# Kernel tuning notes

Measured on AMD Instinct MI355X. Metric: run time of the kernel, lower is better.

The kernel has to match this reference:

```python
import jax, jax.numpy as jnp
import numpy as np

B, T, C, H = 4096, 4, 1024, 8
DH = C // H
SCALE = DH ** -0.5
LN_EPS = 1e-5


def setup_inputs() -> dict:
    key = jax.random.key(0)
    k1, k2, k3 = jax.random.split(key, 3)
    feats = jax.random.normal(k1, (B, T, C), dtype=jnp.float32)
    Wqkv = jax.random.normal(k2, (T, C, 3 * C), dtype=jnp.float32) * 0.02
    bqkv = jnp.zeros((T, 3 * C), dtype=jnp.float32)
    Wproj = jax.random.normal(k3, (T, C, C), dtype=jnp.float32) * 0.02
    bproj = jnp.zeros((T, C), dtype=jnp.float32)
    gamma = jnp.ones((C,), dtype=jnp.float32)
    beta = jnp.zeros((C,), dtype=jnp.float32)
    return {"feats": feats, "Wqkv": Wqkv, "bqkv": bqkv,
            "Wproj": Wproj, "bproj": bproj, "gamma": gamma, "beta": beta}


def reference(feats, Wqkv, bqkv, Wproj, bproj, gamma, beta):
    # Grouped per-task QKV projection: [B,T,C] x [T,C,3C] -> [B,T,3C]
    qkv = jnp.einsum('btc,tcd->btd', feats, Wqkv) + bqkv
    q, k, v = jnp.split(qkv, 3, axis=-1)           # each [B,T,C]
    q = q.reshape(B, T, H, DH)
    k = k.reshape(B, T, H, DH)
    v = v.reshape(B, T, H, DH)
    # Cross-task attention: scores[b, query_task, key_task, head]
    scores = jnp.einsum('bqhd,bkhd->bqkh', q, k) * SCALE
    attn = jax.nn.softmax(scores, axis=2)          # softmax over key-task dim
    ctx = jnp.einsum('bqkh,bkhd->bqhd', attn, v)   # [B,T,H,DH]
    ctx = ctx.reshape(B, T, C)
    # Grouped per-task output projection (dropout is identity in eval)
    ctx = jnp.einsum('btc,tcd->btd', ctx, Wproj) + bproj
    # Residual + shared LayerNorm over channel dim
    x = ctx + feats
    mu = jnp.mean(x, axis=-1, keepdims=True)
    var = jnp.mean(jnp.square(x - mu), axis=-1, keepdims=True)
    return (x - mu) * jax.lax.rsqrt(var + LN_EPS) * gamma + beta
```

## Files before the change

### kernel.cpp

```cpp
#include <hip/hip_runtime.h>
#include <hip/hip_bf16.h>
#include <cstdint>
#include <cstddef>

#define B_SZ 4096
#define T_SZ 4
#define C_SZ 1024
#define H_SZ 8
#define DH_SZ 128
#define NQKV 3072
#define SCALE_F 0.08838834764831845f

typedef float f32x4 __attribute__((ext_vector_type(4)));
typedef short s16x8 __attribute__((ext_vector_type(8)));

static __device__ __forceinline__ float bf2f(unsigned short u) {
    union { unsigned int i; float f; } x; x.i = ((unsigned int)u) << 16; return x.f;
}
static __device__ __forceinline__ unsigned short f2bf(float f) {
    union { unsigned int i; float f; } x; x.f = f;
    unsigned int r = x.i + 0x7FFFu + ((x.i >> 16) & 1u);
    return (unsigned short)(r >> 16);
}

typedef const __attribute__((address_space(1))) void* gas_ptr;
typedef __attribute__((address_space(3))) void* las_ptr;
static __device__ __forceinline__ void async16(const void* g, void* l) {
    __builtin_amdgcn_global_load_lds((gas_ptr)g, (las_ptr)l, 16, 0, 0);
}

__global__ __launch_bounds__(256) void cvt_f32_bf16(const float* __restrict__ src,
                                                    unsigned short* __restrict__ dst, int n4) {
    int stride = gridDim.x * 256;
    for (int i = blockIdx.x * 256 + threadIdx.x; i < n4; i += stride) {
        float4 v = reinterpret_cast<const float4*>(src)[i];
        ushort4 o;
        o.x = f2bf(v.x); o.y = f2bf(v.y); o.z = f2bf(v.z); o.w = f2bf(v.w);
        reinterpret_cast<ushort4*>(dst)[i] = o;
    }
}

__global__ __launch_bounds__(256) void transpose_cvt(const float* __restrict__ src,
                                                     unsigned short* __restrict__ dst,
                                                     int K, int N) {
    __shared__ float tile[64][33];
    const float* s = src + (size_t)blockIdx.z * K * N;
    unsigned short* d = dst + (size_t)blockIdx.z * K * N;
    int n0 = blockIdx.x * 32, k0 = blockIdx.y * 64;
    int tx = threadIdx.x, ty = threadIdx.y;
#pragma unroll
    for (int i = 0; i < 8; i++) {
        int k = k0 + ty + i * 8;
        tile[ty + i * 8][tx] = s[(size_t)k * N + n0 + tx];
    }
    __syncthreads();
#pragma unroll
    for (int i = 0; i < 4; i++) {
        int n = n0 + ty + i * 8;
        ushort2 o;
        o.x = f2bf(tile[2 * tx][ty + i * 8]);
        o.y = f2bf(tile[2 * tx + 1][ty + i * 8]);
        *reinterpret_cast<ushort2*>(&d[(size_t)n * K + k0 + 2 * tx]) = o;
    }
}

template<int NSIZE>
__global__ __launch_bounds__(512, 1) void gemm256(
    const unsigned short* __restrict__ A,
    const unsigned short* __restrict__ Bt,
    const float* __restrict__ bias,
    unsigned short* __restrict__ out_bf)
{
    constexpr int BK  = 64;
    constexpr int NBX = NSIZE / 256;
    constexpr int NBY = B_SZ / 256;
    constexpr int NWG = NBX * NBY * T_SZ;

    __shared__ __align__(16) unsigned short lds[65536];

    const int bid = blockIdx.x;
    const int swz = (bid & 7) * (NWG >> 3) + (bid >> 3);
    const int by  = swz & (NBY - 1);
    const int tmp = swz >> 4;
    const int bx  = tmp % NBX;
    const int t   = tmp / NBX;
    const int m0  = by * 256;
    const int n0  = bx * 256;

    const int tid  = threadIdx.x;
    const int lane = tid & 63;
    const int w    = tid >> 6;
    const int wm   = w >> 2;
    const int wn   = w & 3;
    const int quad = lane >> 4;
    const int l16  = lane & 15;

    const int q0  = w * 128 + lane;
    const int q1  = q0 + 64;
    const int r0  = q0 >> 3, ch0 = (q0 & 7) ^ (r0 & 7);
    const int r1  = q1 >> 3, ch1 = (q1 & 7) ^ (r1 & 7);
    const unsigned short* Abase = A + (size_t)t * C_SZ;
    const unsigned short* Bbase = Bt + (size_t)t * NSIZE * C_SZ;
    const unsigned short* gA0 = Abase + (size_t)(m0 + r0) * (T_SZ * C_SZ) + ch0 * 8;
    const unsigned short* gA1 = Abase + (size_t)(m0 + r1) * (T_SZ * C_SZ) + ch1 * 8;
    const unsigned short* gB0 = Bbase + (size_t)(n0 + r0) * C_SZ + ch0 * 8;
    const unsigned short* gB1 = Bbase + (size_t)(n0 + r1) * C_SZ + ch1 * 8;
    unsigned short* dA0 = &lds[(w * 2 + 0) * 512];
    unsigned short* dA1 = &lds[(w * 2 + 1) * 512];
    unsigned short* dB0 = &lds[32768 + (w * 2 + 0) * 512];
    unsigned short* dB1 = &lds[32768 + (w * 2 + 1) * 512];

#define STG_A(buf, h, kt) do { \
    async16(gA0 + (size_t)(h) * 128 * (T_SZ * C_SZ) + (kt) * BK, dA0 + (buf) * 16384 + (h) * 8192); \
    async16(gA1 + (size_t)(h) * 128 * (T_SZ * C_SZ) + (kt) * BK, dA1 + (buf) * 16384 + (h) * 8192); \
} while (0)
#define STG_B(buf, h, kt) do { \
    async16(gB0 + (size_t)(h) * 128 * C_SZ + (kt) * BK, dB0 + (buf) * 16384 + (h) * 8192); \
    async16(gB1 + (size_t)(h) * 128 * C_SZ + (kt) * BK, dB1 + (buf) * 16384 + (h) * 8192); \
} while (0)

    const int s7   = l16 & 7;
    const int swk0 = ((0 * 4 + quad) ^ s7) * 8;
    const int swk1 = ((1 * 4 + quad) ^ s7) * 8;
    const unsigned short* aR = &lds[wm * 8192 + l16 * 64];
    const unsigned short* bR = &lds[32768 + (wn >> 1) * 8192 + ((wn & 1) * 64 + l16) * 64];

#define LD_A(buf, mh) do { \
    _Pragma("unroll") \
    for (int mi = 0; mi < 4; ++mi) { \
        af[mi][0] = *(const s16x8*)(aR + (buf) * 16384 + ((mh) * 4 + mi) * 1024 + swk0); \
        af[mi][1] = *(const s16x8*)(aR + (buf) * 16384 + ((mh) * 4 + mi) * 1024 + swk1); \
    } \
} while (0)
#define LD_B(buf, nh, dst) do { \
    _Pragma("unroll") \
    for (int ni = 0; ni < 2; ++ni) { \
        dst[ni][0] = *(const s16x8*)(bR + (buf) * 16384 + ((nh) * 2 + ni) * 1024 + swk0); \
        dst[ni][1] = *(const s16x8*)(bR + (buf) * 16384 + ((nh) * 2 + ni) * 1024 + swk1); \
    } \
} while (0)
#define MM(mh, nh, bsrc) do { \
    _Pragma("unroll") \
    for (int mi = 0; mi < 4; ++mi) \
    _Pragma("unroll") \
    for (int ni = 0; ni < 2; ++ni) { \
        acc[(mh) * 4 + mi][(nh) * 2 + ni] = __builtin_amdgcn_mfma_f32_16x16x32_bf16( \
            af[mi][0], bsrc[ni][0], acc[(mh) * 4 + mi][(nh) * 2 + ni], 0, 0, 0); \
        acc[(mh) * 4 + mi][(nh) * 2 + ni] = __builtin_amdgcn_mfma_f32_16x16x32_bf16( \
            af[mi][1], bsrc[ni][1], acc[(mh) * 4 + mi][(nh) * 2 + ni], 0, 0, 0); \
    } \
} while (0)
#define WALL() do { \
    __builtin_amdgcn_s_barrier(); \
    __builtin_amdgcn_sched_barrier(0); \
} while (0)
#define KTILE(buf, kt, SP0, SP23, VMC) do { \
     \
    asm volatile("s_waitcnt vmcnt(" #VMC ")"); \
    __builtin_amdgcn_sched_barrier(0); \
    WALL(); \
    LD_B(buf, 0, bq0); \
    LD_A(buf, 0); \
    LD_B(buf, 1, bq1); \
    if (SP0) STG_A((buf) ^ 1, 1, (kt) + 1); \
    __builtin_amdgcn_s_setprio(1); MM(0, 0, bq0); MM(0, 1, bq1); __builtin_amdgcn_s_setprio(0); \
     \
    WALL(); \
    LD_A(buf, 1); \
    if (SP23) { STG_B(buf, 0, (kt) + 2); STG_A(buf, 0, (kt) + 2); STG_B(buf, 1, (kt) + 2); } \
    __builtin_amdgcn_s_setprio(1); MM(1, 1, bq1); MM(1, 0, bq0); __builtin_amdgcn_s_setprio(0); \
} while (0)

    f32x4 acc[8][4] = {};
    s16x8 af[4][2], bq0[2][2], bq1[2][2];

    STG_A(0, 0, 0); STG_B(0, 0, 0); STG_B(0, 1, 0);
    STG_A(0, 1, 0);
    STG_B(1, 0, 1); STG_A(1, 0, 1); STG_B(1, 1, 1);

#pragma clang loop unroll(disable)
    for (int it = 0; it < 7; ++it) {
        int kt = it * 2;
        KTILE(0, kt,     1, 1, 6);
        KTILE(1, kt + 1, 1, 1, 6);
    }
    KTILE(0, 14, 1, 0, 6);
    KTILE(1, 15, 0, 0, 0);

#undef KTILE
#undef WALL
#undef MM
#undef LD_B
#undef LD_A
#undef STG_B
#undef STG_A

#pragma unroll
    for (int ni = 0; ni < 4; ++ni) {
        int gn = n0 + wn * 64 + ni * 16 + l16;
        float bi = bias[t * NSIZE + gn];
#pragma unroll
        for (int mi = 0; mi < 8; ++mi) {
#pragma unroll
            for (int r = 0; r < 4; ++r) {
                int gm = m0 + wm * 128 + mi * 16 + quad * 4 + r;
                size_t o = (size_t)(gm * T_SZ + t) * NSIZE + gn;
                out_bf[o] = f2bf(acc[mi][ni][r] + bi);
            }
        }
    }
}

__global__ __launch_bounds__(256) void attn_kernel(const unsigned short* __restrict__ qkv,
                                                   unsigned short* __restrict__ ctx) {
    const int tid = threadIdx.x;
    const int li  = tid & 15;
    const int g   = blockIdx.x * 16 + (tid >> 4);
    const int b   = g >> 3, h = g & 7;
    const int d0  = li * 8;

    const unsigned short* base = qkv + (size_t)b * (T_SZ * NQKV) + h * DH_SZ + d0;
    float qf[4][8], kf[4][8], vf[4][8];
#pragma unroll
    for (int i = 0; i < 4; i++) {
        const unsigned short* p = base + (size_t)i * NQKV;
        s16x8 qv = *reinterpret_cast<const s16x8*>(p);
        s16x8 kv = *reinterpret_cast<const s16x8*>(p + C_SZ);
        s16x8 vv = *reinterpret_cast<const s16x8*>(p + 2 * C_SZ);
#pragma unroll
        for (int e = 0; e < 8; e++) {
            qf[i][e] = bf2f((unsigned short)qv[e]);
            kf[i][e] = bf2f((unsigned short)kv[e]);
            vf[i][e] = bf2f((unsigned short)vv[e]);
        }
    }
    float s[4][4];
#pragma unroll
    for (int i = 0; i < 4; i++)
#pragma unroll
        for (int j = 0; j < 4; j++) {
            float p = 0.0f;
#pragma unroll
            for (int e = 0; e < 8; e++) p += qf[i][e] * kf[j][e];
            p += __shfl_xor(p, 8);
            p += __shfl_xor(p, 4);
            p += __shfl_xor(p, 2);
            p += __shfl_xor(p, 1);
            s[i][j] = p * SCALE_F;
        }
#pragma unroll
    for (int i = 0; i < 4; i++) {
        float m = fmaxf(fmaxf(s[i][0], s[i][1]), fmaxf(s[i][2], s[i][3]));
        float e0 = __expf(s[i][0] - m), e1 = __expf(s[i][1] - m);
        float e2 = __expf(s[i][2] - m), e3 = __expf(s[i][3] - m);
        float inv = 1.0f / (e0 + e1 + e2 + e3);
        s[i][0] = e0 * inv; s[i][1] = e1 * inv; s[i][2] = e2 * inv; s[i][3] = e3 * inv;
    }
#pragma unroll
    for (int i = 0; i < 4; i++) {
        s16x8 ov;
#pragma unroll
        for (int e = 0; e < 8; e++) {
            float o = s[i][0] * vf[0][e] + s[i][1] * vf[1][e]
                    + s[i][2] * vf[2][e] + s[i][3] * vf[3][e];
            ov[e] = (short)f2bf(o);
        }
        *reinterpret_cast<s16x8*>(ctx + (size_t)(b * T_SZ + i) * C_SZ + h * DH_SZ + d0) = ov;
    }
}

__global__ __launch_bounds__(256) void ln_fused(const unsigned short* __restrict__ yb,
                                                const float* __restrict__ feats,
                                                const float* __restrict__ gamma,
                                                const float* __restrict__ beta,
                                                float* __restrict__ out) {
    const int wave = threadIdx.x >> 6, lane = threadIdx.x & 63;
    const int row = blockIdx.x * 4 + wave;
    const unsigned short* yp = yb + (size_t)row * C_SZ;
    const float* fp = feats + (size_t)row * C_SZ;

    float x[4][4];
    float s = 0.0f, ss = 0.0f;
#pragma unroll
    for (int c = 0; c < 4; c++) {
        int col = c * 256 + lane * 4;
        ushort4 u = *reinterpret_cast<const ushort4*>(yp + col);
        float4 f = *reinterpret_cast<const float4*>(fp + col);
        x[c][0] = bf2f(u.x) + f.x;
        x[c][1] = bf2f(u.y) + f.y;
        x[c][2] = bf2f(u.z) + f.z;
        x[c][3] = bf2f(u.w) + f.w;
#pragma unroll
        for (int j = 0; j < 4; j++) { s += x[c][j]; ss += x[c][j] * x[c][j]; }
    }
#pragma unroll
    for (int off = 32; off > 0; off >>= 1) { s += __shfl_xor(s, off); ss += __shfl_xor(ss, off); }
    float mean = s * (1.0f / C_SZ);
    float var  = ss * (1.0f / C_SZ) - mean * mean;
    float inv  = rsqrtf(var + 1e-5f);
#pragma unroll
    for (int c = 0; c < 4; c++) {
        int col = c * 256 + lane * 4;
        float4 g  = *reinterpret_cast<const float4*>(gamma + col);
        float4 be = *reinterpret_cast<const float4*>(beta + col);
        float4 o;
        o.x = (x[c][0] - mean) * inv * g.x + be.x;
        o.y = (x[c][1] - mean) * inv * g.y + be.y;
        o.z = (x[c][2] - mean) * inv * g.z + be.z;
        o.w = (x[c][3] - mean) * inv * g.w + be.w;
        *reinterpret_cast<float4*>(out + (size_t)row * C_SZ + col) = o;
    }
}

extern "C" void kernel_launch(void* const* d_in, const int* in_sizes, int n_in,
                              void* d_out, int out_size, void* d_ws, size_t ws_size,
                              hipStream_t stream) {
    const float* feats = (const float*)d_in[0];
    const float* Wqkv  = (const float*)d_in[1];
    const float* bqkv  = (const float*)d_in[2];
    const float* Wproj = (const float*)d_in[3];
    const float* bproj = (const float*)d_in[4];
    const float* gamma = (const float*)d_in[5];
    const float* beta  = (const float*)d_in[6];
    float* out = (float*)d_out;

    char* ws = (char*)d_ws;
    unsigned short* feats_bf = (unsigned short*)(ws);
    unsigned short* wqkv_t   = (unsigned short*)(ws + 33554432);
    unsigned short* wproj_t  = (unsigned short*)(ws + 58720256);
    unsigned short* qkv      = (unsigned short*)(ws + 67108864);
    unsigned short* ctx      = (unsigned short*)(ws + 167772160);
    unsigned short* ybuf_bf  = (unsigned short*)(ws + 67108864);

    cvt_f32_bf16<<<2048, 256, 0, stream>>>(feats, feats_bf, (B_SZ * T_SZ * C_SZ) / 4);
    transpose_cvt<<<dim3(96, 16, 4), dim3(32, 8), 0, stream>>>(Wqkv, wqkv_t, C_SZ, NQKV);
    transpose_cvt<<<dim3(32, 16, 4), dim3(32, 8), 0, stream>>>(Wproj, wproj_t, C_SZ, C_SZ);

    gemm256<NQKV><<<dim3(768), 512, 0, stream>>>(feats_bf, wqkv_t, bqkv, qkv);

    attn_kernel<<<(B_SZ * H_SZ) / 16, 256, 0, stream>>>(qkv, ctx);

    gemm256<C_SZ><<<dim3(256), 512, 0, stream>>>(ctx, wproj_t, bproj, ybuf_bf);

    ln_fused<<<(B_SZ * T_SZ) / 4, 256, 0, stream>>>(ybuf_bf, feats, gamma, beta, out);
}
```

Before: 387.0 us.

## Switch intermediates to task-major layout, stage GEMM epilogue in LDS, merge prep kernels

Intermediate activations (feats bf16, qkv, ctx, projection output) are now stored task-major [T,B,C] instead of [B,T,C], so GEMM A-tile rows are contiguous rather than strided by T*C. The GEMM epilogue writes results to swizzled LDS first and then emits 16-byte vectorized global stores instead of scattered 2-byte stores. The three preprocessing launches (feats convert and two weight transposes) are folded into a single kernel. The attention and LayerNorm kernels get matching index changes, at the cost of an extra LDS round trip and barrier in the epilogue.

```diff
diff --git a/kernel.cpp b/kernel.cpp
--- a/kernel.cpp
+++ b/kernel.cpp
@@ -29,38 +29,57 @@
     __builtin_amdgcn_global_load_lds((gas_ptr)g, (las_ptr)l, 16, 0, 0);
 }
 
-__global__ __launch_bounds__(256) void cvt_f32_bf16(const float* __restrict__ src,
-                                                    unsigned short* __restrict__ dst, int n4) {
-    int stride = gridDim.x * 256;
-    for (int i = blockIdx.x * 256 + threadIdx.x; i < n4; i += stride) {
-        float4 v = reinterpret_cast<const float4*>(src)[i];
-        ushort4 o;
-        o.x = f2bf(v.x); o.y = f2bf(v.y); o.z = f2bf(v.z); o.w = f2bf(v.w);
-        reinterpret_cast<ushort4*>(dst)[i] = o;
-    }
-}
-
-__global__ __launch_bounds__(256) void transpose_cvt(const float* __restrict__ src,
-                                                     unsigned short* __restrict__ dst,
-                                                     int K, int N) {
-    __shared__ float tile[64][33];
-    const float* s = src + (size_t)blockIdx.z * K * N;
-    unsigned short* d = dst + (size_t)blockIdx.z * K * N;
-    int n0 = blockIdx.x * 32, k0 = blockIdx.y * 64;
-    int tx = threadIdx.x, ty = threadIdx.y;
-#pragma unroll
-    for (int i = 0; i < 8; i++) {
-        int k = k0 + ty + i * 8;
-        tile[ty + i * 8][tx] = s[(size_t)k * N + n0 + tx];
-    }
-    __syncthreads();
-#pragma unroll
-    for (int i = 0; i < 4; i++) {
-        int n = n0 + ty + i * 8;
-        ushort2 o;
-        o.x = f2bf(tile[2 * tx][ty + i * 8]);
-        o.y = f2bf(tile[2 * tx + 1][ty + i * 8]);
-        *reinterpret_cast<ushort2*>(&d[(size_t)n * K + k0 + 2 * tx]) = o;
+__global__ __launch_bounds__(256) void prep_kernel(const float* __restrict__ Wqkv,
+                                                   const float* __restrict__ Wproj,
+                                                   const float* __restrict__ feats,
+                                                   unsigned short* __restrict__ wqkvT,
+                                                   unsigned short* __restrict__ wprojT,
+                                                   unsigned short* __restrict__ featsT) {
+    const int bid = blockIdx.x;
+    const int tid = threadIdx.x;
+    if (bid < 8192) {
+        __shared__ float tile[64][33];
+        const float* src; unsigned short* dst; int K = C_SZ, N; int bx, by, bz;
+        if (bid < 6144) {
+            N = NQKV; bx = bid % 96; by = (bid / 96) % 16; bz = bid / 1536;
+            src = Wqkv;  dst = wqkvT;
+        } else {
+            int b2 = bid - 6144;
+            N = C_SZ; bx = b2 % 32; by = (b2 / 32) % 16; bz = b2 / 512;
+            src = Wproj; dst = wprojT;
+        }
+        const float* s = src + (size_t)bz * K * N;
+        unsigned short* d = dst + (size_t)bz * K * N;
+        int n0 = bx * 32, k0 = by * 64;
+        int tx = tid & 31, ty = tid >> 5;
+#pragma unroll
+        for (int i = 0; i < 8; i++) {
+            int k = k0 + ty + i * 8;
+            tile[ty + i * 8][tx] = s[(size_t)k * N + n0 + tx];
+        }
+        __syncthreads();
+#pragma unroll
+        for (int i = 0; i < 4; i++) {
+            int n = n0 + ty + i * 8;
+            ushort2 o;
+            o.x = f2bf(tile[2 * tx][ty + i * 8]);
+            o.y = f2bf(tile[2 * tx + 1][ty + i * 8]);
+            *reinterpret_cast<ushort2*>(&d[(size_t)n * K + k0 + 2 * tx]) = o;
+        }
+    } else {
+        const int wave = tid >> 6, lane = tid & 63;
+        const int r = (bid - 8192) * 4 + wave;
+        const int b = r >> 2, t = r & 3;
+        const float* fp = feats + (size_t)r * C_SZ;
+        unsigned short* op = featsT + ((size_t)t * B_SZ + b) * C_SZ;
+#pragma unroll
+        for (int c = 0; c < 4; c++) {
+            int col = c * 256 + lane * 4;
+            float4 v = *reinterpret_cast<const float4*>(fp + col);
+            ushort4 o;
+            o.x = f2bf(v.x); o.y = f2bf(v.y); o.z = f2bf(v.z); o.w = f2bf(v.w);
+            *reinterpret_cast<ushort4*>(op + col) = o;
+        }
     }
 }
 
@@ -99,10 +118,10 @@
     const int q1  = q0 + 64;
     const int r0  = q0 >> 3, ch0 = (q0 & 7) ^ (r0 & 7);
     const int r1  = q1 >> 3, ch1 = (q1 & 7) ^ (r1 & 7);
-    const unsigned short* Abase = A + (size_t)t * C_SZ;
+    const unsigned short* Abase = A + (size_t)t * B_SZ * C_SZ;
     const unsigned short* Bbase = Bt + (size_t)t * NSIZE * C_SZ;
-    const unsigned short* gA0 = Abase + (size_t)(m0 + r0) * (T_SZ * C_SZ) + ch0 * 8;
-    const unsigned short* gA1 = Abase + (size_t)(m0 + r1) * (T_SZ * C_SZ) + ch1 * 8;
+    const unsigned short* gA0 = Abase + (size_t)(m0 + r0) * C_SZ + ch0 * 8;
+    const unsigned short* gA1 = Abase + (size_t)(m0 + r1) * C_SZ + ch1 * 8;
     const unsigned short* gB0 = Bbase + (size_t)(n0 + r0) * C_SZ + ch0 * 8;
     const unsigned short* gB1 = Bbase + (size_t)(n0 + r1) * C_SZ + ch1 * 8;
     unsigned short* dA0 = &lds[(w * 2 + 0) * 512];
@@ -111,8 +130,8 @@
     unsigned short* dB1 = &lds[32768 + (w * 2 + 1) * 512];
 
 #define STG_A(buf, h, kt) do { \
-    async16(gA0 + (size_t)(h) * 128 * (T_SZ * C_SZ) + (kt) * BK, dA0 + (buf) * 16384 + (h) * 8192); \
-    async16(gA1 + (size_t)(h) * 128 * (T_SZ * C_SZ) + (kt) * BK, dA1 + (buf) * 16384 + (h) * 8192); \
+    async16(gA0 + (size_t)(h) * 128 * C_SZ + (kt) * BK, dA0 + (buf) * 16384 + (h) * 8192); \
+    async16(gA1 + (size_t)(h) * 128 * C_SZ + (kt) * BK, dA1 + (buf) * 16384 + (h) * 8192); \
 } while (0)
 #define STG_B(buf, h, kt) do { \
     async16(gB0 + (size_t)(h) * 128 * C_SZ + (kt) * BK, dB0 + (buf) * 16384 + (h) * 8192); \
@@ -195,19 +214,30 @@
 #undef STG_B
 #undef STG_A
 
+    __syncthreads();
+    unsigned short* ep = &lds[w * 8192];
 #pragma unroll
     for (int ni = 0; ni < 4; ++ni) {
-        int gn = n0 + wn * 64 + ni * 16 + l16;
-        float bi = bias[t * NSIZE + gn];
+        int colb = ni * 16 + l16;
+        float bi = bias[t * NSIZE + n0 + wn * 64 + colb];
 #pragma unroll
         for (int mi = 0; mi < 8; ++mi) {
 #pragma unroll
             for (int r = 0; r < 4; ++r) {
-                int gm = m0 + wm * 128 + mi * 16 + quad * 4 + r;
-                size_t o = (size_t)(gm * T_SZ + t) * NSIZE + gn;
-                out_bf[o] = f2bf(acc[mi][ni][r] + bi);
+                int row = mi * 16 + quad * 4 + r;
+                ep[row * 64 + (colb ^ ((row & 7) << 3))] = f2bf(acc[mi][ni][r] + bi);
             }
         }
+    }
+    const int lr = lane >> 3, lc = lane & 7;
+#pragma unroll
+    for (int j = 0; j < 16; ++j) {
+        int row = j * 8 + lr;
+        s16x8 v = *reinterpret_cast<const s16x8*>(ep + row * 64 + lc * 8);
+        int cdat = (lc ^ (row & 7)) * 8;
+        int gm = m0 + wm * 128 + row;
+        size_t o = ((size_t)t * B_SZ + gm) * NSIZE + (n0 + wn * 64 + cdat);
+        *reinterpret_cast<s16x8*>(out_bf + o) = v;
     }
 }
 
@@ -219,11 +249,10 @@
     const int b   = g >> 3, h = g & 7;
     const int d0  = li * 8;
 
-    const unsigned short* base = qkv + (size_t)b * (T_SZ * NQKV) + h * DH_SZ + d0;
     float qf[4][8], kf[4][8], vf[4][8];
 #pragma unroll
     for (int i = 0; i < 4; i++) {
-        const unsigned short* p = base + (size_t)i * NQKV;
+        const unsigned short* p = qkv + (size_t)i * B_SZ * NQKV + (size_t)b * NQKV + h * DH_SZ + d0;
         s16x8 qv = *reinterpret_cast<const s16x8*>(p);
         s16x8 kv = *reinterpret_cast<const s16x8*>(p + C_SZ);
         s16x8 vv = *reinterpret_cast<const s16x8*>(p + 2 * C_SZ);
@@ -265,7 +294,7 @@
                     + s[i][2] * vf[2][e] + s[i][3] * vf[3][e];
             ov[e] = (short)f2bf(o);
         }
-        *reinterpret_cast<s16x8*>(ctx + (size_t)(b * T_SZ + i) * C_SZ + h * DH_SZ + d0) = ov;
+        *reinterpret_cast<s16x8*>(ctx + (size_t)i * B_SZ * C_SZ + (size_t)b * C_SZ + h * DH_SZ + d0) = ov;
     }
 }
 
@@ -276,7 +305,7 @@
                                                 float* __restrict__ out) {
     const int wave = threadIdx.x >> 6, lane = threadIdx.x & 63;
     const int row = blockIdx.x * 4 + wave;
-    const unsigned short* yp = yb + (size_t)row * C_SZ;
+    const unsigned short* yp = yb + ((size_t)(row & 3) * B_SZ + (row >> 2)) * C_SZ;
     const float* fp = feats + (size_t)row * C_SZ;
 
     float x[4][4];
@@ -332,9 +361,7 @@
     unsigned short* ctx      = (unsigned short*)(ws + 167772160);
     unsigned short* ybuf_bf  = (unsigned short*)(ws + 67108864);
 
-    cvt_f32_bf16<<<2048, 256, 0, stream>>>(feats, feats_bf, (B_SZ * T_SZ * C_SZ) / 4);
-    transpose_cvt<<<dim3(96, 16, 4), dim3(32, 8), 0, stream>>>(Wqkv, wqkv_t, C_SZ, NQKV);
-    transpose_cvt<<<dim3(32, 16, 4), dim3(32, 8), 0, stream>>>(Wproj, wproj_t, C_SZ, C_SZ);
+    prep_kernel<<<12288, 256, 0, stream>>>(Wqkv, Wproj, feats, wqkv_t, wproj_t, feats_bf);
 
     gemm256<NQKV><<<dim3(768), 512, 0, stream>>>(feats_bf, wqkv_t, bqkv, qkv);
 
```

After: 359.7 us. 1.08x faster.
